# Kernel optimization log

Measured on AMD Instinct MI355X. Metric: run time of the kernel, lower is better.

## Reference

```python
import jax, jax.numpy as jnp
import numpy as np

B, C, H, W = 8, 512, 64, 64


def setup_inputs() -> dict:
    key = jax.random.key(0)
    ks = jax.random.split(key, 7)
    s = 1.0 / np.sqrt(C)  # conv2d default init scale
    return {
        "x": jax.random.normal(ks[0], (B, C, H, W), dtype=jnp.float32),
        "wq": jax.random.normal(ks[1], (C, C), dtype=jnp.float32) * s,
        "bq": jax.random.normal(ks[2], (C,), dtype=jnp.float32) * s,
        "wk": jax.random.normal(ks[3], (C, C), dtype=jnp.float32) * s,
        "bk": jax.random.normal(ks[4], (C,), dtype=jnp.float32) * s,
        "wv": jax.random.normal(ks[5], (C, C), dtype=jnp.float32) * s,
        "bv": jax.random.normal(ks[6], (C,), dtype=jnp.float32) * s,
    }


def reference(x, wq, bq, wk, bk, wv, bv):
    b, c, h, w = x.shape
    xf = x.reshape(b, c, h * w)  # (B, C, N)
    # 1x1 convs == per-pixel channel GEMMs
    q = jnp.einsum("oc,bcn->bon", wq, xf) + bq[None, :, None]
    k = jnp.einsum("oc,bcn->bon", wk, xf) + bk[None, :, None]
    v = jnp.einsum("oc,bcn->bon", wv, xf) + bv[None, :, None]
    # channel attention: (B, C, C), contraction over spatial N
    attn = jax.nn.softmax(jnp.einsum("bin,bjn->bij", q, k), axis=-1)
    out = jnp.einsum("bij,bjn->bin", attn, v)
    return out.reshape(b, c, h, w)
```

## Files before the change

kernel.cpp:

```cpp
#include <hip/hip_runtime.h>


typedef unsigned short u16;
typedef short v8s __attribute__((ext_vector_type(8)));
typedef float v4f __attribute__((ext_vector_type(4)));

#define B_ 8
#define C_ 512
#define N_ 4096

__device__ __forceinline__ u16 f2bf(float f) {
  unsigned int u = __builtin_bit_cast(unsigned int, f);
  u = u + 0x7fffu + ((u >> 16) & 1u);
  return (u16)(u >> 16);
}
__device__ __forceinline__ float bf2f(u16 h) {
  unsigned int u = ((unsigned int)h) << 16;
  return __builtin_bit_cast(float, u);
}
__device__ __forceinline__ void gld_lds16(const u16* g, u16* l) {
  __builtin_amdgcn_global_load_lds((__attribute__((address_space(1))) void*)(g),
                                   (__attribute__((address_space(3))) void*)(l),
                                   16, 0, 0);
}

template <bool SPLIT, int EPI, bool TRI>
__global__ __launch_bounds__(256) void gemm_bt(
    const u16* __restrict__ Ah, const u16* __restrict__ Al, long long sA_,
    const u16* __restrict__ Bh, const u16* __restrict__ Bl, long long sB_,
    int K, int Kc, int nsplit, int ldc,
    float* __restrict__ Cf, u16* __restrict__ Ch,
    long long sC_, const float* __restrict__ rowbias) {
  constexpr int NB = SPLIT ? 4 : 2;
  __shared__ __attribute__((aligned(16))) u16 pool[2 * NB * 128 * 32];

  int b, ks, ty_, tx_, tidx;
  if (TRI) {
    int L = (int)blockIdx.z * 10 + (int)blockIdx.x;
    int cpx = (B_ * nsplit * 10) >> 3;
    int Ls = (L & 7) * cpx + (L >> 3);
    int t = Ls % 10, z = Ls / 10;
    b = z / nsplit;
    ks = z % nsplit;
    tidx = t;
    ty_ = (t < 4) ? 0 : (t < 7) ? 1 : (t < 9) ? 2 : 3;
    tx_ = t - ((ty_ == 0) ? 0 : (ty_ == 1) ? 3 : (ty_ == 2) ? 5 : 6);
  } else {
    b = blockIdx.z / nsplit;
    ks = blockIdx.z % nsplit;
    ty_ = blockIdx.y;
    tx_ = blockIdx.x;
    tidx = ty_ * 4 + tx_;
  }
  int tid = threadIdx.x, lane = tid & 63, w = tid >> 6;
  const u16* pAh = Ah + (size_t)b * sA_ + (size_t)ty_ * 128 * K;
  const u16* pBh = Bh + (size_t)b * sB_ + (size_t)tx_ * 128 * K;
  const u16* pAl = SPLIT ? (Al + (size_t)b * sA_ + (size_t)ty_ * 128 * K) : pAh;
  const u16* pBl = SPLIT ? (Bl + (size_t)b * sB_ + (size_t)tx_ * 128 * K) : pBh;
  int wr = (w >> 1) * 64, wc = (w & 1) * 64;
  v4f acc[4][4] = {};

  int srow_off = lane >> 2;
  int gcol = ((lane & 3) ^ ((lane >> 3) & 3)) * 8;

  const u16* sbase;
  int bufsel;
  if (SPLIT) {
    sbase = (w == 0) ? pAh : (w == 1) ? pAl : (w == 2) ? pBh : pBl;
    bufsel = w;
  } else {
    sbase = (w < 2) ? pAh : pBh;
    bufsel = (w >> 1);
  }

  int kbeg = ks * Kc;
  int nIter = Kc >> 5;

  auto STAGE = [&](int pb, int k0) {
    u16* lds = pool + (pb * NB + bufsel) * (128 * 32);
    if constexpr (SPLIT) {
      for (int t = 0; t < 8; ++t)
        gld_lds16(sbase + (size_t)(t * 16 + srow_off) * K + k0 + gcol,
                  lds + t * 16 * 32);
    } else {
      int o = (w & 1) * 4;
      for (int t = 0; t < 4; ++t) {
        int s = o + t;
        gld_lds16(sbase + (size_t)(s * 16 + srow_off) * K + k0 + gcol,
                  lds + s * 16 * 32);
      }
    }
  };

  int r = lane & 15, q = lane >> 4;
  int sw = (q ^ ((r >> 1) & 3)) * 8;

  STAGE(0, kbeg);
  for (int it = 0; it < nIter; ++it) {
    int cur = it & 1;
    bool pf = (it + 1 < nIter);
    if (pf) {
      STAGE(cur ^ 1, kbeg + (it + 1) * 32);
      if constexpr (SPLIT)
        asm volatile("s_waitcnt vmcnt(8)" ::: "memory");
      else
        asm volatile("s_waitcnt vmcnt(4)" ::: "memory");
    } else {
      asm volatile("s_waitcnt vmcnt(0)" ::: "memory");
    }
    __builtin_amdgcn_s_barrier();
    __builtin_amdgcn_sched_barrier(0);

    const u16* base = pool + cur * NB * (128 * 32);
    const u16* A0s = base;
    const u16* A1s = base + 128 * 32;
    const u16* B0s = base + (SPLIT ? 2 : 1) * (128 * 32);
    const u16* B1s = base + 3 * (128 * 32);
    v8s a0[4], a1[4], b0[4], b1[4];
    for (int mt = 0; mt < 4; ++mt) {
      int off = (wr + mt * 16 + r) * 32 + sw;
      a0[mt] = *(const v8s*)(const void*)(A0s + off);
      if (SPLIT) a1[mt] = *(const v8s*)(const void*)(A1s + off);
    }
    for (int nt = 0; nt < 4; ++nt) {
      int off = (wc + nt * 16 + r) * 32 + sw;
      b0[nt] = *(const v8s*)(const void*)(B0s + off);
      if (SPLIT) b1[nt] = *(const v8s*)(const void*)(B1s + off);
    }
    for (int mt = 0; mt < 4; ++mt)
      for (int nt = 0; nt < 4; ++nt) {
        acc[mt][nt] = __builtin_amdgcn_mfma_f32_16x16x32_bf16(a0[mt], b0[nt], acc[mt][nt], 0, 0, 0);
        if (SPLIT) {
          acc[mt][nt] = __builtin_amdgcn_mfma_f32_16x16x32_bf16(a0[mt], b1[nt], acc[mt][nt], 0, 0, 0);
          acc[mt][nt] = __builtin_amdgcn_mfma_f32_16x16x32_bf16(a1[mt], b0[nt], acc[mt][nt], 0, 0, 0);
        }
      }
    asm volatile("" ::: "memory");
    __builtin_amdgcn_s_barrier();
    asm volatile("" ::: "memory");
  }

  if (EPI == 4) {
    constexpr int NT = TRI ? 10 : 16;
    float* dstp = Cf + ((size_t)(b * nsplit + ks) * NT + tidx) * 16384;
    for (int mt = 0; mt < 4; ++mt)
      for (int nt = 0; nt < 4; ++nt) {
        int rl = wr + mt * 16 + q * 4;
        int cl = wc + nt * 16 + r;
        for (int e = 0; e < 4; ++e)
          dstp[(size_t)(rl + e) * 128 + cl] = acc[mt][nt][e];
      }
  } else {
    for (int mt = 0; mt < 4; ++mt)
      for (int nt = 0; nt < 4; ++nt) {
        int row0 = ty_ * 128 + wr + mt * 16 + q * 4;
        int col = tx_ * 128 + wc + nt * 16 + r;
        for (int e = 0; e < 4; ++e) {
          float vv = acc[mt][nt][e];
          size_t off = (size_t)b * sC_ + (size_t)(row0 + e) * ldc + col;
          if (EPI == 2) {
            Ch[off] = f2bf(vv);
          } else {
            Cf[off] = vv + rowbias[(size_t)b * C_ + row0 + e];
          }
        }
      }
  }
}

__global__ __launch_bounds__(256) void conv_split_g(
    const float* __restrict__ P, u16* __restrict__ h, u16* __restrict__ l) {
  __shared__ u16 th[64 * 133];
  __shared__ u16 tl[64 * 133];
  int j = blockIdx.x;
  int b = j & 7;
  int rest = j >> 3;
  int t = rest >> 1;
  int half = rest & 1;
  int rq = (t < 4) ? 0 : (t < 7) ? 1 : (t < 9) ? 2 : 3;
  int cq = t - ((rq == 0) ? 0 : (rq == 1) ? 3 : (rq == 2) ? 5 : 6);
  const float* p0 = P + ((size_t)(b * 8) * 10 + t) * 16384 + (size_t)(half * 64) * 128;
  int tid = threadIdx.x;
  int lr = tid >> 5;
  int c4 = (tid & 31) * 4;
  for (int it = 0; it < 8; ++it) {
    int row = it * 8 + lr;
    const float* pr = p0 + (size_t)row * 128 + c4;
    float v[4] = {0.f, 0.f, 0.f, 0.f};
    for (int ks = 0; ks < 8; ++ks) {
      float4 x = *(const float4*)(pr + (size_t)ks * 10 * 16384);
      v[0] += x.x; v[1] += x.y; v[2] += x.z; v[3] += x.w;
    }
    u16 h4[4], l4[4];
    for (int e = 0; e < 4; ++e) {
      h4[e] = f2bf(v[e]);
      l4[e] = f2bf(v[e] - bf2f(h4[e]));
    }
    int gr = rq * 128 + half * 64 + row, gc = cq * 128 + c4;
    size_t go = ((size_t)b << 18) + (size_t)gr * C_ + gc;
    *(ushort4*)(h + go) = make_ushort4(h4[0], h4[1], h4[2], h4[3]);
    *(ushort4*)(l + go) = make_ushort4(l4[0], l4[1], l4[2], l4[3]);
    for (int e = 0; e < 4; ++e) {
      th[row * 133 + c4 + e] = h4[e];
      tl[row * 133 + c4 + e] = l4[e];
    }
  }
  if (rq == cq) return;
  __syncthreads();
  int orw = tid >> 4;
  int oc4 = (tid & 15) * 4;
  for (int it = 0; it < 8; ++it) {
    int orr = it * 16 + orw;
    u16 h4[4], l4[4];
    for (int e = 0; e < 4; ++e) {
      h4[e] = th[(oc4 + e) * 133 + orr];
      l4[e] = tl[(oc4 + e) * 133 + orr];
    }
    int gr = cq * 128 + orr, gc = rq * 128 + half * 64 + oc4;
    size_t go = ((size_t)b << 18) + (size_t)gr * C_ + gc;
    *(ushort4*)(h + go) = make_ushort4(h4[0], h4[1], h4[2], h4[3]);
    *(ushort4*)(l + go) = make_ushort4(l4[0], l4[1], l4[2], l4[3]);
  }
}

__global__ __launch_bounds__(256) void conv_split(
    const float* __restrict__ P, u16* __restrict__ h, u16* __restrict__ l) {
  size_t i = ((size_t)blockIdx.x * 256 + threadIdx.x) * 4;
  int b = (int)(i >> 18);
  int r = (int)(i >> 9) & 511;
  int c = (int)i & 511;
  int t = (r >> 7) * 4 + (c >> 7);
  const float* p = P + ((size_t)(b * 4) * 16 + t) * 16384 +
                   (size_t)(r & 127) * 128 + (c & 127);
  float v[4] = {0.f, 0.f, 0.f, 0.f};
  for (int ks = 0; ks < 4; ++ks) {
    float4 x0 = *(const float4*)(p + (size_t)ks * 16 * 16384);
    v[0] += x0.x; v[1] += x0.y; v[2] += x0.z; v[3] += x0.w;
  }
  for (int j = 0; j < 4; ++j) {
    u16 hh = f2bf(v[j]);
    h[i + j] = hh;
    l[i + j] = f2bf(v[j] - bf2f(hh));
  }
}

__global__ __launch_bounds__(256) void split_transpose(
    const float* __restrict__ x, u16* __restrict__ xh, u16* __restrict__ xl,
    u16* __restrict__ xhT, float* __restrict__ sx8) {
  __shared__ u16 tile[64 * 66];
  int b = blockIdx.z, ct = blockIdx.y, nt = blockIdx.x;
  int tid = threadIdx.x;
  const float* xb = x + ((size_t)b * C_ + (size_t)ct * 64) * N_ + (size_t)nt * 64;
  float* sxs = sx8 + (size_t)(nt & 7) * (B_ * C_) + b * C_ + ct * 64;
  float4 v4[4];
  for (int it = 0; it < 4; ++it) {
    int idx = it * 1024 + tid * 4;
    v4[it] = *(const float4*)(xb + (size_t)(idx >> 6) * N_ + (idx & 63));
  }
  for (int it = 0; it < 4; ++it) {
    int idx = it * 1024 + tid * 4;
    int cl = idx >> 6;
    int nl = idx & 63;
    float vv[4] = {v4[it].x, v4[it].y, v4[it].z, v4[it].w};
    u16 h4[4], l4[4];
    for (int j = 0; j < 4; ++j) {
      h4[j] = f2bf(vv[j]);
      l4[j] = f2bf(vv[j] - bf2f(h4[j]));
    }
    size_t go = ((size_t)b * C_ + ct * 64 + cl) * N_ + (size_t)nt * 64 + nl;
    *(ushort4*)(xh + go) = make_ushort4(h4[0], h4[1], h4[2], h4[3]);
    *(ushort4*)(xl + go) = make_ushort4(l4[0], l4[1], l4[2], l4[3]);
    for (int j = 0; j < 4; ++j) tile[(nl + j) * 66 + cl] = h4[j];
    float s = vv[0] + vv[1] + vv[2] + vv[3];
    s += __shfl_xor(s, 1); s += __shfl_xor(s, 2);
    s += __shfl_xor(s, 4); s += __shfl_xor(s, 8);
    if ((tid & 15) == 0) atomicAdd(&sxs[cl], s);
  }
  __syncthreads();
  for (int it = 0; it < 4; ++it) {
    int idx = it * 1024 + tid * 4;
    int nr = idx >> 6;
    int c4 = idx & 63;
    const u16* tp = tile + nr * 66 + c4;
    unsigned int lo = *(const unsigned int*)(const void*)(tp);
    unsigned int hi = *(const unsigned int*)(const void*)(tp + 2);
    size_t to = ((size_t)b * N_ + (size_t)nt * 64 + nr) * C_ + ct * 64 + c4;
    *(ushort4*)(xhT + to) = make_ushort4((u16)lo, (u16)(lo >> 16), (u16)hi, (u16)(hi >> 16));
  }
}

__global__ __launch_bounds__(256) void prep_weights(
    const float* __restrict__ wq, const float* __restrict__ wk, const float* __restrict__ wv,
    u16* __restrict__ wqh, u16* __restrict__ wql, u16* __restrict__ wkh,
    u16* __restrict__ wkl, u16* __restrict__ wvT, float* __restrict__ sx8) {
  int idx = blockIdx.x * 256 + threadIdx.x;
  if (blockIdx.x < 128) sx8[idx] = 0.0f;
  float q = wq[idx];
  u16 qh = f2bf(q);
  wqh[idx] = qh;
  wql[idx] = f2bf(q - bf2f(qh));
  float k = wk[idx];
  u16 kh = f2bf(k);
  wkh[idx] = kh;
  wkl[idx] = f2bf(k - bf2f(kh));
  float v = wv[idx];
  wvT[(size_t)(idx & 511) * C_ + (idx >> 9)] = f2bf(v);
}

__global__ __launch_bounds__(256) void bias_vec(
    const float* __restrict__ wq, const float* __restrict__ wk,
    const float* __restrict__ sx8, float* __restrict__ aq, float* __restrict__ ak) {
  int gw = blockIdx.x * 4 + (threadIdx.x >> 6);
  int lane = threadIdx.x & 63;
  int which = gw >> 12;
  int b = (gw >> 9) & 7, i = gw & 511;
  const float* wrow = (which ? wk : wq) + (size_t)i * C_;
  const float* sxb = sx8 + b * C_;
  float s = 0.f;
  for (int c = lane; c < C_; c += 64) {
    float sv = 0.f;
    for (int ss = 0; ss < 8; ++ss) sv += sxb[(size_t)ss * (B_ * C_) + c];
    s += wrow[c] * sv;
  }
  for (int o = 32; o; o >>= 1) s += __shfl_down(s, o);
  if (lane == 0) (which ? ak : aq)[b * C_ + i] = s;
}

__global__ __launch_bounds__(256) void softmax_rows(
    const float* __restrict__ P, const float* __restrict__ aq,
    const float* __restrict__ ak, const float* __restrict__ bq,
    const float* __restrict__ bk, const float* __restrict__ bv,
    u16* __restrict__ attn, float* __restrict__ obias) {
  int row = blockIdx.x * 4 + (threadIdx.x >> 6);
  int lane = threadIdx.x & 63;
  int b = row >> 9, i = row & 511;
  const float* akb = ak + b * C_;
  float aqi = aq[row], bqi = bq[i];
  float lv[8], ev[8];
  float m = -3.4e38f;
  for (int t = 0; t < 8; ++t) {
    int j = t * 64 + lane;
    int tile = (i >> 7) * 4 + (t >> 1);
    size_t base = ((size_t)(b * 4) * 16 + tile) * 16384 +
                  (size_t)(i & 127) * 128 + ((t & 1) * 64 + lane);
    float sv = 0.f;
    for (int ks = 0; ks < 4; ++ks) sv += P[base + (size_t)ks * 16 * 16384];
    float v = sv + aqi * bk[j] + bqi * (akb[j] + 4096.0f * bk[j]);
    lv[t] = v;
    m = fmaxf(m, v);
  }
  for (int o = 32; o; o >>= 1) m = fmaxf(m, __shfl_xor(m, o));
  float se = 0.f, sb = 0.f;
  for (int t = 0; t < 8; ++t) {
    int j = t * 64 + lane;
    float e = expf(lv[t] - m);
    ev[t] = e;
    se += e;
    sb += e * bv[j];
  }
  for (int o = 32; o; o >>= 1) {
    se += __shfl_xor(se, o);
    sb += __shfl_xor(sb, o);
  }
  float inv = 1.0f / se;
  for (int t = 0; t < 8; ++t) attn[(size_t)row * C_ + t * 64 + lane] = f2bf(ev[t] * inv);
  if (lane == 0) obias[row] = sb * inv;
}

extern "C" void kernel_launch(void* const* d_in, const int* in_sizes, int n_in,
                              void* d_out, int out_size, void* d_ws, size_t ws_size,
                              hipStream_t stream) {
  const float* x = (const float*)d_in[0];
  const float* wq = (const float*)d_in[1];
  const float* bq = (const float*)d_in[2];
  const float* wk = (const float*)d_in[3];
  const float* bk = (const float*)d_in[4];
  const float* wv = (const float*)d_in[5];
  const float* bv = (const float*)d_in[6];
  float* out = (float*)d_out;

  const size_t XN = (size_t)B_ * C_ * N_;
  const size_t CCt = (size_t)B_ * C_ * C_;
  const size_t W2 = (size_t)C_ * C_;
  const size_t PARTN = (size_t)B_ * 8 * 10 * 16384;

  u16* XH = (u16*)d_ws;
  u16* XL = XH + XN;
  u16* XHT = XL + XN;
  float* PART = (float*)(XHT + XN);
  u16* GH = (u16*)(PART + PARTN);
  u16* GL = GH + CCt;
  u16* UH = GL + CCt;
  u16* UL = UH + CCt;
  u16* ATTN = UL + CCt;
  u16* MH = ATTN + CCt;
  u16* WQH = MH + CCt;
  u16* WQL = WQH + W2;
  u16* WKH = WQL + W2;
  u16* WKL = WKH + W2;
  u16* WVT = WKL + W2;
  float* SX8 = (float*)(WVT + W2);
  float* AQ = SX8 + 8 * B_ * C_;
  float* AK = AQ + B_ * C_;
  float* OBIAS = AK + B_ * C_;

  prep_weights<<<W2 / 256, 256, 0, stream>>>(wq, wk, wv, WQH, WQL, WKH, WKL, WVT, SX8);
  split_transpose<<<dim3(N_ / 64, C_ / 64, B_), 256, 0, stream>>>(x, XH, XL, XHT, SX8);
  bias_vec<<<2048, 256, 0, stream>>>(wq, wk, SX8, AQ, AK);

  gemm_bt<true, 4, true><<<dim3(10, 1, B_ * 8), 256, 0, stream>>>(
      XH, XL, (long long)((size_t)C_ * N_), XH, XL, (long long)((size_t)C_ * N_),
      N_, 512, 8, C_, PART, nullptr, (long long)W2, nullptr);
  conv_split_g<<<160, 256, 0, stream>>>(PART, GH, GL);

  gemm_bt<true, 4, false><<<dim3(4, 4, B_ * 4), 256, 0, stream>>>(
      WKH, WKL, 0, GH, GL, (long long)W2, C_, 128, 4, C_, PART, nullptr,
      (long long)W2, nullptr);
  conv_split<<<CCt / 1024, 256, 0, stream>>>(PART, UH, UL);

  gemm_bt<true, 4, false><<<dim3(4, 4, B_ * 4), 256, 0, stream>>>(
      WQH, WQL, 0, UH, UL, (long long)W2, C_, 128, 4, C_, PART, nullptr,
      (long long)W2, nullptr);

  softmax_rows<<<(B_ * C_) / 4, 256, 0, stream>>>(PART, AQ, AK, bq, bk, bv, ATTN, OBIAS);

  gemm_bt<false, 2, false><<<dim3(4, 4, B_), 256, 0, stream>>>(
      ATTN, nullptr, (long long)W2, WVT, nullptr, 0, C_, 512, 1, C_, nullptr,
      MH, (long long)W2, nullptr);
  gemm_bt<false, 3, false><<<dim3(N_ / 128, 4, B_), 256, 0, stream>>>(
      MH, nullptr, (long long)W2, XHT, nullptr, (long long)((size_t)N_ * C_),
      C_, 512, 1, N_, out, nullptr, (long long)((size_t)C_ * N_), OBIAS);
}
```

Baseline: 276.5 us.

## Single-buffer lo-part tiles in split GEMM and widen column-sum atomic spread

```diff
diff --git a/kernel.cpp b/kernel.cpp
--- a/kernel.cpp
+++ b/kernel.cpp
@@ -31,8 +31,8 @@
     int K, int Kc, int nsplit, int ldc,
     float* __restrict__ Cf, u16* __restrict__ Ch,
     long long sC_, const float* __restrict__ rowbias) {
-  constexpr int NB = SPLIT ? 4 : 2;
-  __shared__ __attribute__((aligned(16))) u16 pool[2 * NB * 128 * 32];
+  constexpr int NSH = SPLIT ? 6 : 4;
+  __shared__ __attribute__((aligned(16))) u16 pool[NSH * 4096];
 
   int b, ks, ty_, tx_, tidx;
   if (TRI) {
@@ -63,59 +63,67 @@
   int srow_off = lane >> 2;
   int gcol = ((lane & 3) ^ ((lane >> 3) & 3)) * 8;
 
-  const u16* sbase;
-  int bufsel;
-  if (SPLIT) {
-    sbase = (w == 0) ? pAh : (w == 1) ? pAl : (w == 2) ? pBh : pBl;
-    bufsel = w;
-  } else {
-    sbase = (w < 2) ? pAh : pBh;
-    bufsel = (w >> 1);
-  }
-
   int kbeg = ks * Kc;
   int nIter = Kc >> 5;
 
-  auto STAGE = [&](int pb, int k0) {
-    u16* lds = pool + (pb * NB + bufsel) * (128 * 32);
+  auto STAGE_HI = [&](int pb, int k0) {
     if constexpr (SPLIT) {
-      for (int t = 0; t < 8; ++t)
-        gld_lds16(sbase + (size_t)(t * 16 + srow_off) * K + k0 + gcol,
-                  lds + t * 16 * 32);
+      u16* a = pool + pb * 4096;
+      u16* bb = pool + (2 + pb) * 4096;
+      for (int t2 = 0; t2 < 2; ++t2) {
+        int t = w * 2 + t2;
+        gld_lds16(pAh + (size_t)(t * 16 + srow_off) * K + k0 + gcol, a + t * 512);
+        gld_lds16(pBh + (size_t)(t * 16 + srow_off) * K + k0 + gcol, bb + t * 512);
+      }
     } else {
+      u16* lds = pool + pb * 2 * 4096 + (w >> 1) * 4096;
+      const u16* base = (w < 2) ? pAh : pBh;
       int o = (w & 1) * 4;
       for (int t = 0; t < 4; ++t) {
         int s = o + t;
-        gld_lds16(sbase + (size_t)(s * 16 + srow_off) * K + k0 + gcol,
-                  lds + s * 16 * 32);
+        gld_lds16(base + (size_t)(s * 16 + srow_off) * K + k0 + gcol, lds + s * 512);
       }
+    }
+  };
+  auto STAGE_LO = [&](int k0) {
+    u16* a = pool + 4 * 4096;
+    u16* bb = pool + 5 * 4096;
+    for (int t2 = 0; t2 < 2; ++t2) {
+      int t = w * 2 + t2;
+      gld_lds16(pAl + (size_t)(t * 16 + srow_off) * K + k0 + gcol, a + t * 512);
+      gld_lds16(pBl + (size_t)(t * 16 + srow_off) * K + k0 + gcol, bb + t * 512);
     }
   };
 
   int r = lane & 15, q = lane >> 4;
   int sw = (q ^ ((r >> 1) & 3)) * 8;
 
-  STAGE(0, kbeg);
+  STAGE_HI(0, kbeg);
+  if constexpr (SPLIT) STAGE_LO(kbeg);
   for (int it = 0; it < nIter; ++it) {
     int cur = it & 1;
     bool pf = (it + 1 < nIter);
     if (pf) {
-      STAGE(cur ^ 1, kbeg + (it + 1) * 32);
-      if constexpr (SPLIT)
-        asm volatile("s_waitcnt vmcnt(8)" ::: "memory");
-      else
-        asm volatile("s_waitcnt vmcnt(4)" ::: "memory");
+      STAGE_HI(cur ^ 1, kbeg + (it + 1) * 32);
+      asm volatile("s_waitcnt vmcnt(4)" ::: "memory");
     } else {
       asm volatile("s_waitcnt vmcnt(0)" ::: "memory");
     }
     __builtin_amdgcn_s_barrier();
     __builtin_amdgcn_sched_barrier(0);
 
-    const u16* base = pool + cur * NB * (128 * 32);
-    const u16* A0s = base;
-    const u16* A1s = base + 128 * 32;
-    const u16* B0s = base + (SPLIT ? 2 : 1) * (128 * 32);
-    const u16* B1s = base + 3 * (128 * 32);
+    const u16 *A0s, *B0s, *A1s, *B1s;
+    if constexpr (SPLIT) {
+      A0s = pool + cur * 4096;
+      B0s = pool + (2 + cur) * 4096;
+      A1s = pool + 4 * 4096;
+      B1s = pool + 5 * 4096;
+    } else {
+      A0s = pool + cur * 2 * 4096;
+      B0s = A0s + 4096;
+      A1s = A0s;
+      B1s = B0s;
+    }
     v8s a0[4], a1[4], b0[4], b1[4];
     for (int mt = 0; mt < 4; ++mt) {
       int off = (wr + mt * 16 + r) * 32 + sw;
@@ -138,6 +146,7 @@
     asm volatile("" ::: "memory");
     __builtin_amdgcn_s_barrier();
     asm volatile("" ::: "memory");
+    if (SPLIT && pf) STAGE_LO(kbeg + (it + 1) * 32);
   }
 
   if (EPI == 4) {
@@ -246,12 +255,12 @@
 
 __global__ __launch_bounds__(256) void split_transpose(
     const float* __restrict__ x, u16* __restrict__ xh, u16* __restrict__ xl,
-    u16* __restrict__ xhT, float* __restrict__ sx8) {
+    u16* __restrict__ xhT, float* __restrict__ sx16) {
   __shared__ u16 tile[64 * 66];
   int b = blockIdx.z, ct = blockIdx.y, nt = blockIdx.x;
   int tid = threadIdx.x;
   const float* xb = x + ((size_t)b * C_ + (size_t)ct * 64) * N_ + (size_t)nt * 64;
-  float* sxs = sx8 + (size_t)(nt & 7) * (B_ * C_) + b * C_ + ct * 64;
+  float* sxs = sx16 + (size_t)(nt & 15) * (B_ * C_) + b * C_ + ct * 64;
   float4 v4[4];
   for (int it = 0; it < 4; ++it) {
     int idx = it * 1024 + tid * 4;
@@ -276,7 +285,9 @@
     s += __shfl_xor(s, 4); s += __shfl_xor(s, 8);
     if ((tid & 15) == 0) atomicAdd(&sxs[cl], s);
   }
-  __syncthreads();
+  asm volatile("s_waitcnt lgkmcnt(0)" ::: "memory");
+  __builtin_amdgcn_s_barrier();
+  __builtin_amdgcn_sched_barrier(0);
   for (int it = 0; it < 4; ++it) {
     int idx = it * 1024 + tid * 4;
     int nr = idx >> 6;
@@ -292,9 +303,9 @@
 __global__ __launch_bounds__(256) void prep_weights(
     const float* __restrict__ wq, const float* __restrict__ wk, const float* __restrict__ wv,
     u16* __restrict__ wqh, u16* __restrict__ wql, u16* __restrict__ wkh,
-    u16* __restrict__ wkl, u16* __restrict__ wvT, float* __restrict__ sx8) {
+    u16* __restrict__ wkl, u16* __restrict__ wvT, float* __restrict__ sx16) {
   int idx = blockIdx.x * 256 + threadIdx.x;
-  if (blockIdx.x < 128) sx8[idx] = 0.0f;
+  if (blockIdx.x < 256) sx16[idx] = 0.0f;
   float q = wq[idx];
   u16 qh = f2bf(q);
   wqh[idx] = qh;
@@ -309,17 +320,17 @@
 
 __global__ __launch_bounds__(256) void bias_vec(
     const float* __restrict__ wq, const float* __restrict__ wk,
-    const float* __restrict__ sx8, float* __restrict__ aq, float* __restrict__ ak) {
+    const float* __restrict__ sx16, float* __restrict__ aq, float* __restrict__ ak) {
   int gw = blockIdx.x * 4 + (threadIdx.x >> 6);
   int lane = threadIdx.x & 63;
   int which = gw >> 12;
   int b = (gw >> 9) & 7, i = gw & 511;
   const float* wrow = (which ? wk : wq) + (size_t)i * C_;
-  const float* sxb = sx8 + b * C_;
+  const float* sxb = sx16 + b * C_;
   float s = 0.f;
   for (int c = lane; c < C_; c += 64) {
     float sv = 0.f;
-    for (int ss = 0; ss < 8; ++ss) sv += sxb[(size_t)ss * (B_ * C_) + c];
+    for (int ss = 0; ss < 16; ++ss) sv += sxb[(size_t)ss * (B_ * C_) + c];
     s += wrow[c] * sv;
   }
   for (int o = 32; o; o >>= 1) s += __shfl_down(s, o);
@@ -399,14 +410,14 @@
   u16* WKH = WQL + W2;
   u16* WKL = WKH + W2;
   u16* WVT = WKL + W2;
-  float* SX8 = (float*)(WVT + W2);
-  float* AQ = SX8 + 8 * B_ * C_;
+  float* SX16 = (float*)(WVT + W2);
+  float* AQ = SX16 + 16 * B_ * C_;
   float* AK = AQ + B_ * C_;
   float* OBIAS = AK + B_ * C_;
 
-  prep_weights<<<W2 / 256, 256, 0, stream>>>(wq, wk, wv, WQH, WQL, WKH, WKL, WVT, SX8);
-  split_transpose<<<dim3(N_ / 64, C_ / 64, B_), 256, 0, stream>>>(x, XH, XL, XHT, SX8);
-  bias_vec<<<2048, 256, 0, stream>>>(wq, wk, SX8, AQ, AK);
+  prep_weights<<<W2 / 256, 256, 0, stream>>>(wq, wk, wv, WQH, WQL, WKH, WKL, WVT, SX16);
+  split_transpose<<<dim3(N_ / 64, C_ / 64, B_), 256, 0, stream>>>(x, XH, XL, XHT, SX16);
+  bias_vec<<<2048, 256, 0, stream>>>(wq, wk, SX16, AQ, AK);
 
   gemm_bt<true, 4, true><<<dim3(10, 1, B_ * 8), 256, 0, stream>>>(
       XH, XL, (long long)((size_t)C_ * N_), XH, XL, (long long)((size_t)C_ * N_),
```

Result: no change. 280.6 us (+1.5%).
